# Performance work log

Measured on AMD Instinct MI355X. Metric: run time of the kernel, lower is better.

## Reference

```python
import jax, jax.numpy as jnp
import numpy as np

BATCH, AMINOS, ATOMS = 16, 1024, 8192
AMINO_DIM = EMBED_DIM = ATOM_DIM = 128


def setup_inputs() -> dict:
    key = jax.random.key(0)
    ks = jax.random.split(key, 7)
    x = jax.random.normal(ks[0], (BATCH, AMINOS, AMINO_DIM, 3), dtype=jnp.float32)
    embeddings = jax.random.normal(ks[1], (1, ATOMS, EMBED_DIM), dtype=jnp.float32)
    # sorted gather index emulates per-residue expand/concat in aminos_copy
    amino_idx = jnp.sort(jax.random.randint(ks[2], (ATOMS,), 0, AMINOS))
    s_in = 1.0 / np.sqrt(AMINO_DIM)
    s_e = 1.0 / np.sqrt(EMBED_DIM)
    W_emb = jax.random.normal(ks[3], (EMBED_DIM, EMBED_DIM), dtype=jnp.float32) * s_e
    b_emb = jax.random.normal(ks[4], (EMBED_DIM,), dtype=jnp.float32) * s_e
    W_in = jax.random.normal(ks[5], (EMBED_DIM, AMINO_DIM), dtype=jnp.float32) * s_in
    W_out = jax.random.normal(ks[6], (ATOM_DIM, EMBED_DIM), dtype=jnp.float32) * s_e
    return {"x": x, "embeddings": embeddings, "amino_idx": amino_idx,
            "W_emb": W_emb, "b_emb": b_emb, "W_in": W_in, "W_out": W_out}


def reference(x, embeddings, amino_idx, W_emb, b_emb, W_in, W_out):
    # modulation = lin_embed(embeddings): (1, atoms, E)
    mod = jnp.einsum('oae,fe->oaf', embeddings, W_emb) + b_emb
    # lin_in over channel dim, independent of vector index: (b, aminos, E, 3)
    h = jnp.einsum('bacv,ec->baev', x, W_in)
    # aminos_copy as a single gather along the amino axis -> (b, atoms, E, 3)
    g = jnp.take(h, amino_idx, axis=1)
    # modulate (broadcast modulation over batch and vector index)
    y = mod[..., None] * g
    # lin_out over channel dim: (b, atoms, atom_dim, 3)
    return jnp.einsum('baev,de->badv', y, W_out)
```

## Files before the change

### kernel.cpp

```cpp
#include <hip/hip_runtime.h>
#include <hip/hip_bf16.h>

#define AMINOS 1024
#define ATOMS  8192

typedef __attribute__((ext_vector_type(8))) short  short8;
typedef __attribute__((ext_vector_type(4))) float  f32x4;

__device__ __forceinline__ unsigned short f2bf(float f) {
    unsigned int u; __builtin_memcpy(&u, &f, 4);
    unsigned int r = (u + 0x7fffu + ((u >> 16) & 1u)) >> 16;
    return (unsigned short)r;
}
__device__ __forceinline__ float bf2f(unsigned short us) {
    unsigned int x = ((unsigned int)us) << 16;
    float f; __builtin_memcpy(&f, &x, 4);
    return f;
}

__device__ __forceinline__ int swz(int row, int ch) { return row * 16 + (ch ^ (row & 7)); }

__global__ __launch_bounds__(256) void k_convert(const float* __restrict__ wemb,
                                                 const float* __restrict__ win,
                                                 const float* __restrict__ wout,
                                                 unsigned short* __restrict__ dst) {
    int i = blockIdx.x * 256 + threadIdx.x;
    const float* src = (i < 16384) ? wemb : ((i < 32768) ? win : wout);
    dst[i] = f2bf(src[i & 16383]);
}

__global__ __launch_bounds__(256) void k_mod(const float* __restrict__ emb,
                                             const unsigned short* __restrict__ wembB,
                                             const float* __restrict__ bemb,
                                             float* __restrict__ mod) {
    __shared__ short Al[64 * 128];
    __shared__ short Bl[128 * 128];
    const int tid = threadIdx.x;
    const int a0 = blockIdx.x * 64;

    #pragma unroll
    for (int t = 0; t < 4; ++t) {
        int task = tid + t * 256;
        int row = task >> 4, ch = task & 15;
        const f32x4* p = (const f32x4*)(emb + (a0 + row) * 128 + ch * 8);
        f32x4 lo = p[0], hi = p[1];
        short8 v;
        v[0]=f2bf(lo[0]); v[1]=f2bf(lo[1]); v[2]=f2bf(lo[2]); v[3]=f2bf(lo[3]);
        v[4]=f2bf(hi[0]); v[5]=f2bf(hi[1]); v[6]=f2bf(hi[2]); v[7]=f2bf(hi[3]);
        *(short8*)&Al[swz(row, ch) * 8] = v;
    }
    #pragma unroll
    for (int t = 0; t < 8; ++t) {
        int cc = tid + t * 256;
        int rr = cc >> 4, ch = cc & 15;
        short8 v = *(const short8*)(wembB + cc * 8);
        *(short8*)&Bl[swz(rr, ch) * 8] = v;
    }
    __syncthreads();

    const int lane = tid & 63, w = tid >> 6;
    const int col = lane & 15, kg = lane >> 4;
    const int rt = w;

    short8 af[4];
    #pragma unroll
    for (int ks = 0; ks < 4; ++ks) af[ks] = *(const short8*)&Al[swz(rt * 16 + col, ks * 4 + kg) * 8];

    f32x4 acc[8];
    #pragma unroll
    for (int ct = 0; ct < 8; ++ct) { acc[ct][0]=0.f; acc[ct][1]=0.f; acc[ct][2]=0.f; acc[ct][3]=0.f; }

    #pragma unroll
    for (int ct = 0; ct < 8; ++ct) {
        int r = ct * 16 + col;
        #pragma unroll
        for (int ks = 0; ks < 4; ++ks) {
            short8 bf = *(const short8*)&Bl[swz(r, ks * 4 + kg) * 8];
            acc[ct] = __builtin_amdgcn_mfma_f32_16x16x32_bf16(af[ks], bf, acc[ct], 0, 0, 0);
        }
    }
    #pragma unroll
    for (int ct = 0; ct < 8; ++ct) {
        int f = ct * 16 + col;
        float bb = bemb[f];
        #pragma unroll
        for (int reg = 0; reg < 4; ++reg) {
            int r = rt * 16 + kg * 4 + reg;
            mod[(a0 + r) * 128 + f] = acc[ct][reg] + bb;
        }
    }
}

__global__ __launch_bounds__(256) void k_h(const float* __restrict__ x,
                                           const unsigned short* __restrict__ winB,
                                           unsigned short* __restrict__ h) {
    __shared__ short Al[48 * 128];
    __shared__ short Bl[128 * 128];
    unsigned short* Hs = (unsigned short*)Bl;
    const int tid = threadIdx.x;

    #pragma unroll
    for (int t = 0; t < 8; ++t) {
        int cc = tid + t * 256;
        int rr = cc >> 4, ch = cc & 15;
        short8 v = *(const short8*)(winB + cc * 8);
        *(short8*)&Bl[swz(rr, ch) * 8] = v;
    }
    __syncthreads();

    const int lane = tid & 63, w = tid >> 6;
    const int col = lane & 15, kg = lane >> 4;

    short8 bfr[2][4];
    #pragma unroll
    for (int c2 = 0; c2 < 2; ++c2) {
        int r = (w * 2 + c2) * 16 + col;
        #pragma unroll
        for (int ks = 0; ks < 4; ++ks) bfr[c2][ks] = *(const short8*)&Bl[swz(r, ks * 4 + kg) * 8];
    }

    for (int it = 0; it < 4; ++it) {
        const int g0 = blockIdx.x * 64 + it * 16;
        {
            int p = tid >> 4, ch = tid & 15;
            const f32x4* q = (const f32x4*)(x + (size_t)(g0 + p) * 384 + ch * 24);
            f32x4 q0 = q[0], q1 = q[1], q2 = q[2], q3 = q[3], q4 = q[4], q5 = q[5];
            float e[24];
            *(f32x4*)&e[0]  = q0; *(f32x4*)&e[4]  = q1; *(f32x4*)&e[8]  = q2;
            *(f32x4*)&e[12] = q3; *(f32x4*)&e[16] = q4; *(f32x4*)&e[20] = q5;
            #pragma unroll
            for (int v = 0; v < 3; ++v) {
                short8 vv;
                #pragma unroll
                for (int i = 0; i < 8; ++i) vv[i] = (short)f2bf(e[v + 3 * i]);
                *(short8*)&Al[swz(p * 3 + v, ch) * 8] = vv;
            }
        }
        __syncthreads();

        f32x4 acc[3][2];
        #pragma unroll
        for (int rt = 0; rt < 3; ++rt)
            #pragma unroll
            for (int c2 = 0; c2 < 2; ++c2) { acc[rt][c2][0]=0.f; acc[rt][c2][1]=0.f; acc[rt][c2][2]=0.f; acc[rt][c2][3]=0.f; }

        #pragma unroll
        for (int rt = 0; rt < 3; ++rt) {
            int r = rt * 16 + col;
            short8 af[4];
            #pragma unroll
            for (int ks = 0; ks < 4; ++ks) af[ks] = *(const short8*)&Al[swz(r, ks * 4 + kg) * 8];
            #pragma unroll
            for (int ks = 0; ks < 4; ++ks)
                #pragma unroll
                for (int c2 = 0; c2 < 2; ++c2)
                    acc[rt][c2] = __builtin_amdgcn_mfma_f32_16x16x32_bf16(af[ks], bfr[c2][ks], acc[rt][c2], 0, 0, 0);
        }
        __syncthreads();

        #pragma unroll
        for (int rt = 0; rt < 3; ++rt)
            #pragma unroll
            for (int c2 = 0; c2 < 2; ++c2) {
                int e = (w * 2 + c2) * 16 + col;
                #pragma unroll
                for (int reg = 0; reg < 4; ++reg) {
                    int R = rt * 16 + kg * 4 + reg;
                    Hs[R * 128 + e] = f2bf(acc[rt][c2][reg]);
                }
            }
        __syncthreads();

        unsigned short* hb = h + (size_t)g0 * 3 * 128;
        #pragma unroll
        for (int t2 = 0; t2 < 3; ++t2) {
            int c = tid + t2 * 256;
            *(short8*)(hb + c * 8) = *(const short8*)&Hs[c * 8];
        }
        __syncthreads();
    }
}

__global__ __launch_bounds__(256) void k_out(const unsigned short* __restrict__ h,
                                             const float* __restrict__ mod,
                                             const int* __restrict__ idx,
                                             const unsigned short* __restrict__ woutB,
                                             float* __restrict__ out) {
    __shared__ short Al[48 * 128];
    __shared__ short Bl[128 * 128];
    float* Os = (float*)Bl;
    const int tid = threadIdx.x;
    const int b = blockIdx.x & 15;
    const int abase = (blockIdx.x >> 4) * 64;

    #pragma unroll
    for (int t = 0; t < 8; ++t) {
        int cc = tid + t * 256;
        int rr = cc >> 4, ch = cc & 15;
        short8 v = *(const short8*)(woutB + cc * 8);
        *(short8*)&Bl[swz(rr, ch) * 8] = v;
    }
    __syncthreads();

    const int lane = tid & 63, w = tid >> 6;
    const int col = lane & 15, kg = lane >> 4;

    short8 bfr[2][4];
    #pragma unroll
    for (int c2 = 0; c2 < 2; ++c2) {
        int r = (w * 2 + c2) * 16 + col;
        #pragma unroll
        for (int ks = 0; ks < 4; ++ks) bfr[c2][ks] = *(const short8*)&Bl[swz(r, ks * 4 + kg) * 8];
    }

    for (int it = 0; it < 4; ++it) {
        const int a0 = abase + it * 16;
        #pragma unroll
        for (int t = 0; t < 3; ++t) {
            int task = tid + t * 256;
            int row = task >> 4, ch = task & 15;
            int al = row / 3, v = row - 3 * al;
            int a = a0 + al;
            int ia = idx[a];
            short8 hv = *(const short8*)(h + (size_t)((b * AMINOS + ia) * 3 + v) * 128 + ch * 8);
            const f32x4* mp = (const f32x4*)(mod + a * 128 + ch * 8);
            f32x4 m0 = mp[0], m1 = mp[1];
            short8 vv;
            vv[0]=(short)f2bf(bf2f((unsigned short)hv[0]) * m0[0]);
            vv[1]=(short)f2bf(bf2f((unsigned short)hv[1]) * m0[1]);
            vv[2]=(short)f2bf(bf2f((unsigned short)hv[2]) * m0[2]);
            vv[3]=(short)f2bf(bf2f((unsigned short)hv[3]) * m0[3]);
            vv[4]=(short)f2bf(bf2f((unsigned short)hv[4]) * m1[0]);
            vv[5]=(short)f2bf(bf2f((unsigned short)hv[5]) * m1[1]);
            vv[6]=(short)f2bf(bf2f((unsigned short)hv[6]) * m1[2]);
            vv[7]=(short)f2bf(bf2f((unsigned short)hv[7]) * m1[3]);
            *(short8*)&Al[swz(row, ch) * 8] = vv;
        }
        __syncthreads();

        f32x4 acc[3][2];
        #pragma unroll
        for (int rt = 0; rt < 3; ++rt)
            #pragma unroll
            for (int c2 = 0; c2 < 2; ++c2) { acc[rt][c2][0]=0.f; acc[rt][c2][1]=0.f; acc[rt][c2][2]=0.f; acc[rt][c2][3]=0.f; }

        #pragma unroll
        for (int rt = 0; rt < 3; ++rt) {
            int r = rt * 16 + col;
            short8 af[4];
            #pragma unroll
            for (int ks = 0; ks < 4; ++ks) af[ks] = *(const short8*)&Al[swz(r, ks * 4 + kg) * 8];
            #pragma unroll
            for (int ks = 0; ks < 4; ++ks)
                #pragma unroll
                for (int c2 = 0; c2 < 2; ++c2)
                    acc[rt][c2] = __builtin_amdgcn_mfma_f32_16x16x32_bf16(af[ks], bfr[c2][ks], acc[rt][c2], 0, 0, 0);
        }
        __syncthreads();

        #pragma unroll
        for (int rt = 0; rt < 3; ++rt)
            #pragma unroll
            for (int c2 = 0; c2 < 2; ++c2) {
                int d = (w * 2 + c2) * 16 + col;
                #pragma unroll
                for (int reg = 0; reg < 4; ++reg) {
                    int R = rt * 16 + kg * 4 + reg;
                    int al = R / 3, v = R - 3 * al;
                    Os[al * 384 + d * 3 + v] = acc[rt][c2][reg];
                }
            }
        __syncthreads();

        float* ob = out + ((size_t)b * ATOMS + a0) * 384;
        #pragma unroll
        for (int t2 = 0; t2 < 6; ++t2) {
            int c = tid + t2 * 256;
            *(f32x4*)(ob + c * 4) = *(const f32x4*)&Os[c * 4];
        }
        __syncthreads();
    }
}

extern "C" void kernel_launch(void* const* d_in, const int* in_sizes, int n_in,
                              void* d_out, int out_size, void* d_ws, size_t ws_size,
                              hipStream_t stream) {
    const float* x    = (const float*)d_in[0];
    const float* emb  = (const float*)d_in[1];
    const int*   idx  = (const int*)d_in[2];
    const float* wemb = (const float*)d_in[3];
    const float* bemb = (const float*)d_in[4];
    const float* win  = (const float*)d_in[5];
    const float* wout = (const float*)d_in[6];
    float* out = (float*)d_out;

    char* ws = (char*)d_ws;
    float*          mod = (float*)ws;
    unsigned short* h   = (unsigned short*)(ws + (4u << 20));
    unsigned short* wB  = (unsigned short*)(ws + 16777216u);

    k_convert<<<192, 256, 0, stream>>>(wemb, win, wout, wB);
    k_mod    <<<128, 256, 0, stream>>>(emb, wB, bemb, mod);
    k_h      <<<256, 256, 0, stream>>>(x, wB + 16384, h);
    k_out    <<<2048, 256, 0, stream>>>(h, mod, idx, wB + 32768, out);
}
```

Measured before the change: 245.4 us.

## Merge weight conversion and pre-stages into one kernel, stream output non-temporally

```diff
diff --git a/kernel.cpp b/kernel.cpp
--- a/kernel.cpp
+++ b/kernel.cpp
@@ -20,198 +20,178 @@
 
 __device__ __forceinline__ int swz(int row, int ch) { return row * 16 + (ch ^ (row & 7)); }
 
-__global__ __launch_bounds__(256) void k_convert(const float* __restrict__ wemb,
-                                                 const float* __restrict__ win,
-                                                 const float* __restrict__ wout,
-                                                 unsigned short* __restrict__ dst) {
-    int i = blockIdx.x * 256 + threadIdx.x;
-    const float* src = (i < 16384) ? wemb : ((i < 32768) ? win : wout);
-    dst[i] = f2bf(src[i & 16383]);
-}
-
-__global__ __launch_bounds__(256) void k_mod(const float* __restrict__ emb,
-                                             const unsigned short* __restrict__ wembB,
-                                             const float* __restrict__ bemb,
-                                             float* __restrict__ mod) {
-    __shared__ short Al[64 * 128];
-    __shared__ short Bl[128 * 128];
-    const int tid = threadIdx.x;
-    const int a0 = blockIdx.x * 64;
-
-    #pragma unroll
-    for (int t = 0; t < 4; ++t) {
-        int task = tid + t * 256;
-        int row = task >> 4, ch = task & 15;
-        const f32x4* p = (const f32x4*)(emb + (a0 + row) * 128 + ch * 8);
-        f32x4 lo = p[0], hi = p[1];
-        short8 v;
-        v[0]=f2bf(lo[0]); v[1]=f2bf(lo[1]); v[2]=f2bf(lo[2]); v[3]=f2bf(lo[3]);
-        v[4]=f2bf(hi[0]); v[5]=f2bf(hi[1]); v[6]=f2bf(hi[2]); v[7]=f2bf(hi[3]);
-        *(short8*)&Al[swz(row, ch) * 8] = v;
-    }
+__device__ __forceinline__ void stage_w_f32(const float* __restrict__ W, short* Bl, int tid) {
     #pragma unroll
     for (int t = 0; t < 8; ++t) {
         int cc = tid + t * 256;
         int rr = cc >> 4, ch = cc & 15;
-        short8 v = *(const short8*)(wembB + cc * 8);
+        const f32x4* p = (const f32x4*)(W + cc * 8);
+        f32x4 lo = p[0], hi = p[1];
+        short8 v;
+        v[0]=(short)f2bf(lo[0]); v[1]=(short)f2bf(lo[1]); v[2]=(short)f2bf(lo[2]); v[3]=(short)f2bf(lo[3]);
+        v[4]=(short)f2bf(hi[0]); v[5]=(short)f2bf(hi[1]); v[6]=(short)f2bf(hi[2]); v[7]=(short)f2bf(hi[3]);
         *(short8*)&Bl[swz(rr, ch) * 8] = v;
     }
-    __syncthreads();
-
+}
+
+__global__ __launch_bounds__(256) void k_pre(const float* __restrict__ emb,
+                                             const float* __restrict__ wemb,
+                                             const float* __restrict__ bemb,
+                                             const float* __restrict__ x,
+                                             const float* __restrict__ win,
+                                             float* __restrict__ mod,
+                                             unsigned short* __restrict__ h) {
+    __shared__ short Al[64 * 128];
+    __shared__ short Bl[128 * 128];
+    const int tid = threadIdx.x;
     const int lane = tid & 63, w = tid >> 6;
     const int col = lane & 15, kg = lane >> 4;
-    const int rt = w;
-
-    short8 af[4];
-    #pragma unroll
-    for (int ks = 0; ks < 4; ++ks) af[ks] = *(const short8*)&Al[swz(rt * 16 + col, ks * 4 + kg) * 8];
-
-    f32x4 acc[8];
-    #pragma unroll
-    for (int ct = 0; ct < 8; ++ct) { acc[ct][0]=0.f; acc[ct][1]=0.f; acc[ct][2]=0.f; acc[ct][3]=0.f; }
-
-    #pragma unroll
-    for (int ct = 0; ct < 8; ++ct) {
-        int r = ct * 16 + col;
-        #pragma unroll
-        for (int ks = 0; ks < 4; ++ks) {
-            short8 bf = *(const short8*)&Bl[swz(r, ks * 4 + kg) * 8];
-            acc[ct] = __builtin_amdgcn_mfma_f32_16x16x32_bf16(af[ks], bf, acc[ct], 0, 0, 0);
-        }
-    }
-    #pragma unroll
-    for (int ct = 0; ct < 8; ++ct) {
-        int f = ct * 16 + col;
-        float bb = bemb[f];
-        #pragma unroll
-        for (int reg = 0; reg < 4; ++reg) {
-            int r = rt * 16 + kg * 4 + reg;
-            mod[(a0 + r) * 128 + f] = acc[ct][reg] + bb;
-        }
-    }
-}
-
-__global__ __launch_bounds__(256) void k_h(const float* __restrict__ x,
-                                           const unsigned short* __restrict__ winB,
-                                           unsigned short* __restrict__ h) {
-    __shared__ short Al[48 * 128];
-    __shared__ short Bl[128 * 128];
-    unsigned short* Hs = (unsigned short*)Bl;
+
+    if (blockIdx.x < 128) {
+        const int a0 = blockIdx.x * 64;
+        #pragma unroll
+        for (int t = 0; t < 4; ++t) {
+            int task = tid + t * 256;
+            int row = task >> 4, ch = task & 15;
+            const f32x4* p = (const f32x4*)(emb + (row + a0) * 128 + ch * 8);
+            f32x4 lo = p[0], hi = p[1];
+            short8 v;
+            v[0]=(short)f2bf(lo[0]); v[1]=(short)f2bf(lo[1]); v[2]=(short)f2bf(lo[2]); v[3]=(short)f2bf(lo[3]);
+            v[4]=(short)f2bf(hi[0]); v[5]=(short)f2bf(hi[1]); v[6]=(short)f2bf(hi[2]); v[7]=(short)f2bf(hi[3]);
+            *(short8*)&Al[swz(row, ch) * 8] = v;
+        }
+        stage_w_f32(wemb, Bl, tid);
+        __syncthreads();
+
+        const int rt = w;
+        short8 af[4];
+        #pragma unroll
+        for (int ks = 0; ks < 4; ++ks) af[ks] = *(const short8*)&Al[swz(rt * 16 + col, ks * 4 + kg) * 8];
+
+        f32x4 acc[8];
+        #pragma unroll
+        for (int ct = 0; ct < 8; ++ct) { acc[ct][0]=0.f; acc[ct][1]=0.f; acc[ct][2]=0.f; acc[ct][3]=0.f; }
+
+        #pragma unroll
+        for (int ct = 0; ct < 8; ++ct) {
+            int r = ct * 16 + col;
+            #pragma unroll
+            for (int ks = 0; ks < 4; ++ks) {
+                short8 bf = *(const short8*)&Bl[swz(r, ks * 4 + kg) * 8];
+                acc[ct] = __builtin_amdgcn_mfma_f32_16x16x32_bf16(af[ks], bf, acc[ct], 0, 0, 0);
+            }
+        }
+        #pragma unroll
+        for (int ct = 0; ct < 8; ++ct) {
+            int f = ct * 16 + col;
+            float bb = bemb[f];
+            #pragma unroll
+            for (int reg = 0; reg < 4; ++reg) {
+                int r = rt * 16 + kg * 4 + reg;
+                mod[(a0 + r) * 128 + f] = acc[ct][reg] + bb;
+            }
+        }
+    } else {
+        unsigned short* Hs = (unsigned short*)Bl;
+        stage_w_f32(win, Bl, tid);
+        __syncthreads();
+
+        short8 bfr[2][4];
+        #pragma unroll
+        for (int c2 = 0; c2 < 2; ++c2) {
+            int r = (w * 2 + c2) * 16 + col;
+            #pragma unroll
+            for (int ks = 0; ks < 4; ++ks) bfr[c2][ks] = *(const short8*)&Bl[swz(r, ks * 4 + kg) * 8];
+        }
+
+        for (int it = 0; it < 4; ++it) {
+            const int g0 = (blockIdx.x - 128) * 64 + it * 16;
+            {
+                int p = tid >> 4, ch = tid & 15;
+                const f32x4* q = (const f32x4*)(x + (size_t)(g0 + p) * 384 + ch * 24);
+                f32x4 q0 = q[0], q1 = q[1], q2 = q[2], q3 = q[3], q4 = q[4], q5 = q[5];
+                float e[24];
+                *(f32x4*)&e[0]  = q0; *(f32x4*)&e[4]  = q1; *(f32x4*)&e[8]  = q2;
+                *(f32x4*)&e[12] = q3; *(f32x4*)&e[16] = q4; *(f32x4*)&e[20] = q5;
+                #pragma unroll
+                for (int v = 0; v < 3; ++v) {
+                    short8 vv;
+                    #pragma unroll
+                    for (int i = 0; i < 8; ++i) vv[i] = (short)f2bf(e[v + 3 * i]);
+                    *(short8*)&Al[swz(p * 3 + v, ch) * 8] = vv;
+                }
+            }
+            __syncthreads();
+
+            f32x4 acc[3][2];
+            #pragma unroll
+            for (int rt = 0; rt < 3; ++rt)
+                #pragma unroll
+                for (int c2 = 0; c2 < 2; ++c2) { acc[rt][c2][0]=0.f; acc[rt][c2][1]=0.f; acc[rt][c2][2]=0.f; acc[rt][c2][3]=0.f; }
+
+            #pragma unroll
+            for (int rt = 0; rt < 3; ++rt) {
+                int r = rt * 16 + col;
+                short8 af[4];
+                #pragma unroll
+                for (int ks = 0; ks < 4; ++ks) af[ks] = *(const short8*)&Al[swz(r, ks * 4 + kg) * 8];
+                #pragma unroll
+                for (int ks = 0; ks < 4; ++ks)
+                    #pragma unroll
+                    for (int c2 = 0; c2 < 2; ++c2)
+                        acc[rt][c2] = __builtin_amdgcn_mfma_f32_16x16x32_bf16(af[ks], bfr[c2][ks], acc[rt][c2], 0, 0, 0);
+            }
+            __syncthreads();
+
+            #pragma unroll
+            for (int rt = 0; rt < 3; ++rt)
+                #pragma unroll
+                for (int c2 = 0; c2 < 2; ++c2) {
+                    int e = (w * 2 + c2) * 16 + col;
+                    #pragma unroll
+                    for (int reg = 0; reg < 4; ++reg) {
+                        int R = rt * 16 + kg * 4 + reg;
+                        Hs[R * 128 + e] = f2bf(acc[rt][c2][reg]);
+                    }
+                }
+            __syncthreads();
+
+            unsigned short* hb = h + (size_t)g0 * 3 * 128;
+            #pragma unroll
+            for (int t2 = 0; t2 < 3; ++t2) {
+                int c = tid + t2 * 256;
+                *(short8*)(hb + c * 8) = *(const short8*)&Hs[c * 8];
+            }
+            __syncthreads();
+        }
+    }
+}
+
+__global__ __launch_bounds__(256) void k_out(const unsigned short* __restrict__ h,
+                                             const float* __restrict__ mod,
+                                             const int* __restrict__ idx,
+                                             const float* __restrict__ wout,
+                                             float* __restrict__ out) {
+    __shared__ short L[18432];
     const int tid = threadIdx.x;
-
-    #pragma unroll
-    for (int t = 0; t < 8; ++t) {
-        int cc = tid + t * 256;
-        int rr = cc >> 4, ch = cc & 15;
-        short8 v = *(const short8*)(winB + cc * 8);
-        *(short8*)&Bl[swz(rr, ch) * 8] = v;
-    }
-    __syncthreads();
-
+    const int b = blockIdx.x & 15;
+    const int abase = (blockIdx.x >> 4) * 64;
     const int lane = tid & 63, w = tid >> 6;
     const int col = lane & 15, kg = lane >> 4;
 
+    stage_w_f32(wout, L, tid);
+    __syncthreads();
     short8 bfr[2][4];
     #pragma unroll
     for (int c2 = 0; c2 < 2; ++c2) {
         int r = (w * 2 + c2) * 16 + col;
         #pragma unroll
-        for (int ks = 0; ks < 4; ++ks) bfr[c2][ks] = *(const short8*)&Bl[swz(r, ks * 4 + kg) * 8];
-    }
-
-    for (int it = 0; it < 4; ++it) {
-        const int g0 = blockIdx.x * 64 + it * 16;
-        {
-            int p = tid >> 4, ch = tid & 15;
-            const f32x4* q = (const f32x4*)(x + (size_t)(g0 + p) * 384 + ch * 24);
-            f32x4 q0 = q[0], q1 = q[1], q2 = q[2], q3 = q[3], q4 = q[4], q5 = q[5];
-            float e[24];
-            *(f32x4*)&e[0]  = q0; *(f32x4*)&e[4]  = q1; *(f32x4*)&e[8]  = q2;
-            *(f32x4*)&e[12] = q3; *(f32x4*)&e[16] = q4; *(f32x4*)&e[20] = q5;
-            #pragma unroll
-            for (int v = 0; v < 3; ++v) {
-                short8 vv;
-                #pragma unroll
-                for (int i = 0; i < 8; ++i) vv[i] = (short)f2bf(e[v + 3 * i]);
-                *(short8*)&Al[swz(p * 3 + v, ch) * 8] = vv;
-            }
-        }
-        __syncthreads();
-
-        f32x4 acc[3][2];
-        #pragma unroll
-        for (int rt = 0; rt < 3; ++rt)
-            #pragma unroll
-            for (int c2 = 0; c2 < 2; ++c2) { acc[rt][c2][0]=0.f; acc[rt][c2][1]=0.f; acc[rt][c2][2]=0.f; acc[rt][c2][3]=0.f; }
-
-        #pragma unroll
-        for (int rt = 0; rt < 3; ++rt) {
-            int r = rt * 16 + col;
-            short8 af[4];
-            #pragma unroll
-            for (int ks = 0; ks < 4; ++ks) af[ks] = *(const short8*)&Al[swz(r, ks * 4 + kg) * 8];
-            #pragma unroll
-            for (int ks = 0; ks < 4; ++ks)
-                #pragma unroll
-                for (int c2 = 0; c2 < 2; ++c2)
-                    acc[rt][c2] = __builtin_amdgcn_mfma_f32_16x16x32_bf16(af[ks], bfr[c2][ks], acc[rt][c2], 0, 0, 0);
-        }
-        __syncthreads();
-
-        #pragma unroll
-        for (int rt = 0; rt < 3; ++rt)
-            #pragma unroll
-            for (int c2 = 0; c2 < 2; ++c2) {
-                int e = (w * 2 + c2) * 16 + col;
-                #pragma unroll
-                for (int reg = 0; reg < 4; ++reg) {
-                    int R = rt * 16 + kg * 4 + reg;
-                    Hs[R * 128 + e] = f2bf(acc[rt][c2][reg]);
-                }
-            }
-        __syncthreads();
-
-        unsigned short* hb = h + (size_t)g0 * 3 * 128;
-        #pragma unroll
-        for (int t2 = 0; t2 < 3; ++t2) {
-            int c = tid + t2 * 256;
-            *(short8*)(hb + c * 8) = *(const short8*)&Hs[c * 8];
-        }
-        __syncthreads();
-    }
-}
-
-__global__ __launch_bounds__(256) void k_out(const unsigned short* __restrict__ h,
-                                             const float* __restrict__ mod,
-                                             const int* __restrict__ idx,
-                                             const unsigned short* __restrict__ woutB,
-                                             float* __restrict__ out) {
-    __shared__ short Al[48 * 128];
-    __shared__ short Bl[128 * 128];
-    float* Os = (float*)Bl;
-    const int tid = threadIdx.x;
-    const int b = blockIdx.x & 15;
-    const int abase = (blockIdx.x >> 4) * 64;
-
-    #pragma unroll
-    for (int t = 0; t < 8; ++t) {
-        int cc = tid + t * 256;
-        int rr = cc >> 4, ch = cc & 15;
-        short8 v = *(const short8*)(woutB + cc * 8);
-        *(short8*)&Bl[swz(rr, ch) * 8] = v;
+        for (int ks = 0; ks < 4; ++ks) bfr[c2][ks] = *(const short8*)&L[swz(r, ks * 4 + kg) * 8];
     }
     __syncthreads();
 
-    const int lane = tid & 63, w = tid >> 6;
-    const int col = lane & 15, kg = lane >> 4;
-
-    short8 bfr[2][4];
-    #pragma unroll
-    for (int c2 = 0; c2 < 2; ++c2) {
-        int r = (w * 2 + c2) * 16 + col;
-        #pragma unroll
-        for (int ks = 0; ks < 4; ++ks) bfr[c2][ks] = *(const short8*)&Bl[swz(r, ks * 4 + kg) * 8];
-    }
+    short* Al = L;
+    float* Os = (float*)(L + 6144);
 
     for (int it = 0; it < 4; ++it) {
         const int a0 = abase + it * 16;
@@ -276,7 +256,8 @@
         #pragma unroll
         for (int t2 = 0; t2 < 6; ++t2) {
             int c = tid + t2 * 256;
-            *(f32x4*)(ob + c * 4) = *(const f32x4*)&Os[c * 4];
+            f32x4 vv = *(const f32x4*)&Os[c * 4];
+            __builtin_nontemporal_store(vv, (f32x4*)(ob + c * 4));
         }
         __syncthreads();
     }
@@ -297,10 +278,7 @@
     char* ws = (char*)d_ws;
     float*          mod = (float*)ws;
     unsigned short* h   = (unsigned short*)(ws + (4u << 20));
-    unsigned short* wB  = (unsigned short*)(ws + 16777216u);
-
-    k_convert<<<192, 256, 0, stream>>>(wemb, win, wout, wB);
-    k_mod    <<<128, 256, 0, stream>>>(emb, wB, bemb, mod);
-    k_h      <<<256, 256, 0, stream>>>(x, wB + 16384, h);
-    k_out    <<<2048, 256, 0, stream>>>(h, mod, idx, wB + 32768, out);
-}
+
+    k_pre<<<384, 256, 0, stream>>>(emb, wemb, bemb, x, win, mod, h);
+    k_out<<<2048, 256, 0, stream>>>(h, mod, idx, wout, out);
+}
```

After: 245.3 us. Within noise of the previous version (-0.0%).
